# Optimization experiments

Hardware: AMD Instinct MI355X
Metric: run time of the kernel (lower is better)

The kernel has to match this reference:

```python
import jax, jax.numpy as jnp
import numpy as np

N = 20000; E = 320000; G = 64; C_IN = 128; H = 128; L = 3; S = 4
EPS = 1e-5; SLOPE = 0.01  # GraphNorm eps, leaky_relu negative slope


def _kruskal(ei, ew, n):
    # Kruskal MST over edges sorted by usage-count weight; returns bidirectional MST edges
    # and the updated usage counts (used edges get +1), mirroring kruskal_mst_track_usage.
    order = np.argsort(ew, kind='stable')
    s = ei[0][order]; d = ei[1][order]
    parent = np.arange(n)
    def find(u):
        while parent[u] != u:
            parent[u] = parent[parent[u]]
            u = parent[u]
        return u
    mst = []; used = []
    for i in range(s.shape[0]):
        ru = find(s[i]); rv = find(d[i])
        if ru != rv:
            parent[ru] = rv
            mst.append((s[i], d[i]))
            used.append(order[i])
            if len(mst) == n - 1:
                break
    ew = ew.copy(); ew[np.asarray(used)] += 1
    m = np.asarray(mst, dtype=np.int64).T  # [2, ~n-1]
    return np.concatenate([m, m[::-1]], axis=1), ew  # bidirectional


def setup_inputs():
    rng = np.random.default_rng(0)
    x = rng.standard_normal((N, C_IN), dtype=np.float32)
    edge_index = rng.integers(0, N, size=(2, E)).astype(np.int64)
    batch = np.sort(rng.integers(0, G, size=N)).astype(np.int64)
    # split_graph: shuffle edges, then repeatedly extract MSTs (no_grad / CPU in original)
    perm = rng.permutation(E)
    ei_p = edge_index[:, perm]
    ew = np.zeros(E, dtype=np.int64)
    msts = []
    for _ in range(S - 1):  # only splits 0..3 are used; split 0 is the shuffled full graph
        m, ew = _kruskal(ei_p, ew, N)
        msts.append(m)
    def gp(shape):
        return jnp.asarray((0.05 * rng.standard_normal(shape)).astype(np.float32))
    return {
        'x': jnp.asarray(x),
        'emb_W': gp((C_IN, H)), 'emb_b': gp((H,)),
        'main_W': gp((L, H, H)), 'main_b': gp((L, H)),
        'main_gw': jnp.ones((L, H), jnp.float32), 'main_gb': jnp.zeros((L, H), jnp.float32), 'main_gms': jnp.ones((L, H), jnp.float32),
        'loc_W': gp((L, H, H)), 'loc_b': gp((L, H)),
        'loc_gw': jnp.ones((L, H), jnp.float32), 'loc_gb': jnp.zeros((L, H), jnp.float32), 'loc_gms': jnp.ones((L, H), jnp.float32),
        'merge_W': gp((H * (S + 1), H)), 'merge_b': gp((H,)),
        'edge_index': jnp.asarray(edge_index),
        'edges0': jnp.asarray(ei_p),
        'edges1': jnp.asarray(msts[0]),
        'edges2': jnp.asarray(msts[1]),
        'edges3': jnp.asarray(msts[2]),
        'batch': jnp.asarray(batch),
    }


def _seg(v, idx, n):
    return jax.ops.segment_sum(v, idx, num_segments=n)


def _gcn(x, W, b, src, dst):
    # PyG GCNConv with self-loops and symmetric normalization
    n = x.shape[0]
    h = x @ W
    deg = _seg(jnp.ones(src.shape[0], x.dtype), dst, n) + 1.0
    dinv = jax.lax.rsqrt(deg)
    coef = (dinv[src] * dinv[dst])[:, None]
    out = _seg(h[src] * coef, dst, n) + h * (dinv * dinv)[:, None]  # neighbors + self-loop
    return out + b


def _graph_norm(x, batch, cnt, w, b, ms):
    # PyG GraphNorm: per-graph mean with learnable mean_scale, per-graph variance
    mean = _seg(x, batch, G) / cnt
    out = x - ms * mean[batch]
    var = _seg(out * out, batch, G) / cnt
    inv = jax.lax.rsqrt(var + EPS)
    return w * out * inv[batch] + b


def _gnn(x, src, dst, Ws, bs, gw, gb, gms, batch, cnt):
    hist = []
    for l in range(L):
        x = _gcn(x, Ws[l], bs[l], src, dst)
        x = _graph_norm(x, batch, cnt, gw[l], gb[l], gms[l])
        x = jax.nn.leaky_relu(x, SLOPE)
        hist.append(x)  # dropout in eval mode = identity
    return hist


def _forward(x, emb_W, emb_b, main_W, main_b, main_gw, main_gb, main_gms,
             loc_W, loc_b, loc_gw, loc_gb, loc_gms, merge_W, merge_b,
             edge_index, edges0, edges1, edges2, edges3, batch):
    cnt = jnp.maximum(_seg(jnp.ones(N, x.dtype), batch, G), 1.0)[:, None]  # [G,1]
    h = x @ emb_W + emb_b
    main_hist = _gnn(h, edge_index[0], edge_index[1], main_W, main_b, main_gw, main_gb, main_gms, batch, cnt)
    split_hists = [_gnn(h, e[0], e[1], loc_W, loc_b, loc_gw, loc_gb, loc_gms, batch, cnt)
                   for e in (edges0, edges1, edges2, edges3)]
    gs = []
    for l in range(L):
        xl = jnp.concatenate([sh[l] for sh in split_hists] + [main_hist[l]], axis=1)  # [N, 5H]
        xl = xl @ merge_W + merge_b
        gs.append(_seg(xl, batch, G) / cnt)  # global_mean_pool
    return jnp.mean(jnp.stack(gs), axis=0)  # [G, H]


def reference(x, emb_W, emb_b, main_W, main_b, main_gw, main_gb, main_gms,
              loc_W, loc_b, loc_gw, loc_gb, loc_gms, merge_W, merge_b,
              edge_index, edges0, edges1, edges2, edges3, batch):
    return _forward(x, emb_W, emb_b, main_W, main_b, main_gw, main_gb, main_gms,
                    loc_W, loc_b, loc_gw, loc_gb, loc_gms, merge_W, merge_b,
                    edge_index, edges0, edges1, edges2, edges3, batch)
```

## Files before the change

### kernel.cpp

```cpp
#include <hip/hip_runtime.h>

#define NN 20000
#define NNP 20032
#define NH 128
#define NG 64
#define NLAY 3
#define NCH 5
#define GEPS 1e-5f
#define GSLOPE 0.01f

typedef unsigned short u16;
typedef unsigned int u32;
typedef __attribute__((ext_vector_type(8))) short short8;
typedef __attribute__((ext_vector_type(4))) float float4v;
typedef __attribute__((ext_vector_type(2))) float f32x2;

__device__ __forceinline__ u16 f2bf(float f) {
  union { float f; u32 u; } v; v.f = f;
  u32 r = (v.u + 0x7fffu + ((v.u >> 16) & 1u)) >> 16;
  return (u16)r;
}

struct ZP {
  const u16* A[NCH];
  const u16* W[NCH];
  u16* Y[NCH];
  int ystride[NCH];
  u16* Xo[NCH];
  u16* Xn[NCH];
  const float* bias[NCH];
  const float* gw[NCH];
  const float* gb[NCH];
  const float* gms[NCH];
  int colbase[NCH];
};

struct ES4 {
  const int* e[4];
  int cnt[4];
  int off[4];
};


__global__ void k_deg(ES4 es, int* __restrict__ deg) {
  int s = blockIdx.y;
  int i = blockIdx.x * 256 + threadIdx.x;
  int E = es.cnt[s];
  if (i < E) atomicAdd(&deg[s * NN + es.e[s][E + i]], 1);
}

__global__ __launch_bounds__(1024) void k_scan(const int* __restrict__ deg,
                                               int* __restrict__ indptr,
                                               int* __restrict__ cursor,
                                               float* __restrict__ dinv,
                                               const int* __restrict__ batch,
                                               int* __restrict__ counts,
                                               int* __restrict__ gstart) {
  int s = blockIdx.x;
  int t = threadIdx.x;
  if (s == 4) {
    int g = t;
    if (g < NG) {
      auto lb = [&](int key) {
        int lo = 0, hi = NN;
        while (lo < hi) {
          int mid = (lo + hi) >> 1;
          if (batch[mid] < key) lo = mid + 1; else hi = mid;
        }
        return lo;
      };
      int a = lb(g), b = lb(g + 1);
      gstart[g] = a;
      counts[g] = b - a;
    }
    return;
  }
  const int* d = deg + s * NN;
  int* ip = indptr + s * (NN + 1);
  int* cu = cursor + s * (NN + 1);
  int lane = t & 63, wv = t >> 6;
  __shared__ int wsum[16];
  int run = 0;
  const int NT = (NN + 1023) / 1024;
  for (int tile = 0; tile < NT; tile++) {
    int idx = tile * 1024 + t;
    int v = 0;
    if (idx < NN) {
      v = d[idx];
      dinv[s * NN + idx] = rsqrtf((float)v + 1.0f);
    }
    int x = v;
#pragma unroll
    for (int o = 1; o < 64; o <<= 1) {
      int y = __shfl_up(x, o);
      if (lane >= o) x += y;
    }
    if (lane == 63) wsum[wv] = x;
    __syncthreads();
    if (wv == 0) {
      int y = (lane < 16) ? wsum[lane] : 0;
#pragma unroll
      for (int o = 1; o < 16; o <<= 1) {
        int z = __shfl_up(y, o);
        if (lane >= o) y += z;
      }
      if (lane < 16) wsum[lane] = y;
    }
    __syncthreads();
    int waveoff = (wv == 0) ? 0 : wsum[wv - 1];
    int excl = run + waveoff + x - v;
    if (idx < NN) { ip[idx] = excl; cu[idx] = excl; }
    run += wsum[15];
    __syncthreads();
  }
  if (t == 0) { ip[NN] = run; cu[NN] = run; }
}

__global__ void k_fill(ES4 es, const float* __restrict__ dinv, int* __restrict__ cursor,
                       int2* __restrict__ ent) {
  int s = blockIdx.y;
  int i = blockIdx.x * 256 + threadIdx.x;
  int E = es.cnt[s];
  if (i >= E) return;
  int src = es.e[s][i];
  int dst = es.e[s][E + i];
  int pos = atomicAdd(&cursor[s * (NN + 1) + dst], 1);
  float c = dinv[s * NN + src] * dinv[s * NN + dst];
  ent[es.off[s] + pos] = make_int2(src, __float_as_int(c));
}

__global__ __launch_bounds__(256) void k_prep(const float* __restrict__ embW,
                                              const float* __restrict__ locW,
                                              const float* __restrict__ mainW,
                                              u16* __restrict__ wt,
                                              const float* __restrict__ x,
                                              u16* __restrict__ xb) {
  int ybk = blockIdx.y;
  if (ybk == 7) {
    int i = (blockIdx.x * 256 + threadIdx.x) * 8;
    if (i >= NN * NH) return;
    float4 a = *(const float4*)(x + i);
    float4 b = *(const float4*)(x + i + 4);
    uint4 o;
    o.x = f2bf(a.x) | ((u32)f2bf(a.y) << 16);
    o.y = f2bf(a.z) | ((u32)f2bf(a.w) << 16);
    o.z = f2bf(b.x) | ((u32)f2bf(b.y) << 16);
    o.w = f2bf(b.z) | ((u32)f2bf(b.w) << 16);
    *(uint4*)(xb + i) = o;
    return;
  }
  if (blockIdx.x >= 16) return;
  int mat = ybk;
  const float* W = (mat == 0) ? embW : ((mat <= 3) ? locW + (mat - 1) * NH * NH
                                                   : mainW + (mat - 4) * NH * NH);
  int tile = blockIdx.x;
  int tk = (tile >> 2) * 32;
  int tn = (tile & 3) * 32;
  __shared__ float tl[32][33];
  int c = threadIdx.x & 31, r = threadIdx.x >> 5;
#pragma unroll
  for (int rr = 0; rr < 32; rr += 8)
    tl[r + rr][c] = W[(size_t)(tk + r + rr) * NH + tn + c];
  __syncthreads();
#pragma unroll
  for (int rr = 0; rr < 32; rr += 8)
    wt[(size_t)mat * NH * NH + (size_t)(tn + r + rr) * NH + tk + c] = f2bf(tl[c][r + rr]);
}


__global__ __launch_bounds__(256) void k_gemm_bf(ZP p, const float* __restrict__ gbias) {
  int zi = blockIdx.y;
  const u16* __restrict__ A = p.A[zi];
  const u16* __restrict__ Wt = p.W[zi];
  u16* __restrict__ Y = p.Y[zi];
  int yst = p.ystride[zi];
  __shared__ u16 As[64][136];
  __shared__ u16 Bs[128][136];
  int t = threadIdx.x;
  int row0 = blockIdx.x * 64;
  int c = t & 15, rs = t >> 4;
#pragma unroll
  for (int pass = 0; pass < 4; pass++) {
    int r = pass * 16 + rs;
    *(uint4*)(&As[r][c * 8]) = *(const uint4*)(A + (size_t)(row0 + r) * NH + c * 8);
  }
#pragma unroll
  for (int pass = 0; pass < 8; pass++) {
    int n = pass * 16 + rs;
    *(uint4*)(&Bs[n][c * 8]) = *(const uint4*)(Wt + (size_t)n * NH + c * 8);
  }
  __syncthreads();
  int lane = t & 63, w = t >> 6;
  int m16 = lane & 15, quad = lane >> 4;
  float4v acc[8];
#pragma unroll
  for (int i = 0; i < 8; i++) acc[i] = (float4v)(0.f);
#pragma unroll
  for (int kk = 0; kk < 4; kk++) {
    short8 av = *(const short8*)(&As[w * 16 + m16][kk * 32 + quad * 8]);
#pragma unroll
    for (int ct = 0; ct < 8; ct++) {
      short8 bv = *(const short8*)(&Bs[ct * 16 + m16][kk * 32 + quad * 8]);
      acc[ct] = __builtin_amdgcn_mfma_f32_16x16x32_bf16(av, bv, acc[ct], 0, 0, 0);
    }
  }
  __syncthreads();
#pragma unroll
  for (int ct = 0; ct < 8; ct++) {
    float bv = gbias ? gbias[ct * 16 + m16] : 0.f;
#pragma unroll
    for (int r = 0; r < 4; r++) {
      As[w * 16 + quad * 4 + r][ct * 16 + m16] = f2bf(acc[ct][r] + bv);
    }
  }
  __syncthreads();
#pragma unroll
  for (int pass = 0; pass < 4; pass++) {
    int r = pass * 16 + rs;
    int gr = row0 + r;
    if (gr < NN) *(uint4*)(Y + (size_t)gr * yst + c * 8) = *(const uint4*)(&As[r][c * 8]);
  }
}

__device__ __forceinline__ f32x2 bf2x2(u32 v) {
  f32x2 r;
  r.x = __uint_as_float(v << 16);
  r.y = __uint_as_float(v & 0xffff0000u);
  return r;
}

__device__ __forceinline__ void fma8p(f32x2* a, uint4 v, float cf) {
  f32x2 c2; c2.x = cf; c2.y = cf;
  a[0] += c2 * bf2x2(v.x);
  a[1] += c2 * bf2x2(v.y);
  a[2] += c2 * bf2x2(v.z);
  a[3] += c2 * bf2x2(v.w);
}

__device__ __forceinline__ void fin_chain(const float* a, const u16* Yb, int st, int node,
                                          int fo, float d2, const float* bias,
                                          u16* __restrict__ Xo) {
  uint4 sv = *(const uint4*)(Yb + (size_t)node * st + fo);
  float s[8] = {
    __uint_as_float(sv.x << 16), __uint_as_float(sv.x & 0xffff0000u),
    __uint_as_float(sv.y << 16), __uint_as_float(sv.y & 0xffff0000u),
    __uint_as_float(sv.z << 16), __uint_as_float(sv.z & 0xffff0000u),
    __uint_as_float(sv.w << 16), __uint_as_float(sv.w & 0xffff0000u)};
  float4 b0 = *(const float4*)(bias + fo);
  float4 b1 = *(const float4*)(bias + fo + 4);
  float bb[8] = {b0.x, b0.y, b0.z, b0.w, b1.x, b1.y, b1.z, b1.w};
  float o[8];
#pragma unroll
  for (int j = 0; j < 8; j++) o[j] = a[j] + d2 * s[j] + bb[j];
  uint4 ou;
  u32* op = (u32*)&ou;
#pragma unroll
  for (int j = 0; j < 4; j++)
    op[j] = (u32)f2bf(o[2 * j]) | ((u32)f2bf(o[2 * j + 1]) << 16);
  *(uint4*)(Xo + (size_t)node * NH + fo) = ou;
}

__global__ __launch_bounds__(256) void k_agg2(ZP p, const int* __restrict__ indptr,
                                              const int2* __restrict__ ent,
                                              const float* __restrict__ dinv, int4 entoff) {
  int y = blockIdx.y;
  int wv = threadIdx.x >> 6, lane = threadIdx.x & 63;
  int g = lane >> 4;
  int fo = (lane & 15) * 8;
  if (y == 0) {
    int node = blockIdx.x * 4 + wv;
    if (node >= NN) return;
    int beg = indptr[node], end = indptr[node + 1];
    const u16* __restrict__ Y0 = p.Y[0];
    const u16* __restrict__ Y4 = p.Y[4];
    int st = p.ystride[0];
    f32x2 a0[4], a4[4];
#pragma unroll
    for (int j = 0; j < 4; j++) { a0[j] = (f32x2)(0.f); a4[j] = (f32x2)(0.f); }
    int e = beg + g;
    for (; e + 4 < end; e += 8) {
      int2 sa = ent[e];
      int2 sb = ent[e + 4];
      size_t ra = (size_t)sa.x * st + fo;
      size_t rb = (size_t)sb.x * st + fo;
      uint4 va0 = *(const uint4*)(Y0 + ra);
      uint4 va4 = *(const uint4*)(Y4 + ra);
      uint4 vb0 = *(const uint4*)(Y0 + rb);
      uint4 vb4 = *(const uint4*)(Y4 + rb);
      float ca = __int_as_float(sa.y), cb = __int_as_float(sb.y);
      fma8p(a0, va0, ca); fma8p(a4, va4, ca);
      fma8p(a0, vb0, cb); fma8p(a4, vb4, cb);
    }
    if (e < end) {
      int2 sc = ent[e];
      float cf = __int_as_float(sc.y);
      size_t ro = (size_t)sc.x * st + fo;
      uint4 v0 = *(const uint4*)(Y0 + ro);
      uint4 v4 = *(const uint4*)(Y4 + ro);
      fma8p(a0, v0, cf);
      fma8p(a4, v4, cf);
    }
    float* f0 = (float*)a0;
    float* f4 = (float*)a4;
#pragma unroll
    for (int j = 0; j < 8; j++) {
      f0[j] += __shfl_xor(f0[j], 16);
      f0[j] += __shfl_xor(f0[j], 32);
      f4[j] += __shfl_xor(f4[j], 16);
      f4[j] += __shfl_xor(f4[j], 32);
    }
    if (g == 0) {
      float di = dinv[node];
      float d2 = di * di;
      fin_chain(f0, Y0, st, node, fo, d2, p.bias[0], p.Xo[0]);
      fin_chain(f4, Y4, st, node, fo, d2, p.bias[4], p.Xo[4]);
    }
  } else {
    int node = blockIdx.x * 16 + wv * 4 + g;
    if (node >= NN) return;
    int s = y;
    const int* ip = indptr + s * (NN + 1);
    int eb = (s == 1) ? entoff.y : ((s == 2) ? entoff.z : entoff.w);
    const u16* __restrict__ Y = p.Y[y];
    int st = p.ystride[y];
    int beg = ip[node], end = ip[node + 1];
    const int2* __restrict__ ev = ent + eb;
    f32x2 a[4];
#pragma unroll
    for (int j = 0; j < 4; j++) a[j] = (f32x2)(0.f);
    for (int e = beg; e < end; e++) {
      int2 sc = ev[e];
      uint4 v = *(const uint4*)(Y + (size_t)sc.x * st + fo);
      fma8p(a, v, __int_as_float(sc.y));
    }
    float di = dinv[s * NN + node];
    float d2 = di * di;
    fin_chain((float*)a, Y, st, node, fo, d2, p.bias[y], p.Xo[y]);
  }
}

__global__ __launch_bounds__(256) void k_norm2(ZP p, const int* __restrict__ gstart,
                                               const int* __restrict__ counts,
                                               float* __restrict__ Ml) {
  int g = blockIdx.x, zi = blockIdx.y, fc = blockIdx.z;
  const u16* __restrict__ X = p.Xo[zi];
  u16* __restrict__ Xn = p.Xn[zi];
  int t = threadIdx.x;
  int fj = t & 15;
  int f2 = fc * 32 + fj * 2;
  int rh = t >> 4;
  int start = gstart[g], cnt = counts[g];
  __shared__ float red[4][16][17];
  float s0 = 0.f, s1 = 0.f, q0 = 0.f, q1 = 0.f;
  for (int i = rh; i < cnt; i += 16) {
    u32 v = *(const u32*)(X + (size_t)(start + i) * NH + f2);
    float v0 = __uint_as_float(v << 16), v1 = __uint_as_float(v & 0xffff0000u);
    s0 += v0; q0 += v0 * v0;
    s1 += v1; q1 += v1 * v1;
  }
  red[0][rh][fj] = s0; red[1][rh][fj] = s1;
  red[2][rh][fj] = q0; red[3][rh][fj] = q1;
  __syncthreads();
#pragma unroll
  for (int off = 8; off >= 1; off >>= 1) {
    if (rh < off) {
      red[0][rh][fj] += red[0][rh + off][fj];
      red[1][rh][fj] += red[1][rh + off][fj];
      red[2][rh][fj] += red[2][rh + off][fj];
      red[3][rh][fj] += red[3][rh + off][fj];
    }
    __syncthreads();
  }
  float cntf = fmaxf((float)cnt, 1.f);
  float w0 = p.gw[zi][f2], w1 = p.gw[zi][f2 + 1];
  float b0 = p.gb[zi][f2], b1 = p.gb[zi][f2 + 1];
  float ms0 = p.gms[zi][f2], ms1 = p.gms[zi][f2 + 1];
  float mean0 = red[0][0][fj] / cntf, mean1 = red[1][0][fj] / cntf;
  float var0 = red[2][0][fj] / cntf - (2.f * ms0 - ms0 * ms0) * mean0 * mean0;
  float var1 = red[3][0][fj] / cntf - (2.f * ms1 - ms1 * ms1) * mean1 * mean1;
  float inv0 = rsqrtf(var0 + GEPS), inv1 = rsqrtf(var1 + GEPS);
  __syncthreads();
  float m0 = 0.f, m1 = 0.f;
  for (int i = rh; i < cnt; i += 16) {
    size_t ro = (size_t)(start + i) * NH + f2;
    u32 v = *(const u32*)(X + ro);
    float v0 = __uint_as_float(v << 16), v1 = __uint_as_float(v & 0xffff0000u);
    float o0 = w0 * (v0 - ms0 * mean0) * inv0 + b0;
    float o1 = w1 * (v1 - ms1 * mean1) * inv1 + b1;
    o0 = (o0 >= 0.f) ? o0 : GSLOPE * o0;
    o1 = (o1 >= 0.f) ? o1 : GSLOPE * o1;
    if (Xn) *(u32*)(Xn + ro) = (u32)f2bf(o0) | ((u32)f2bf(o1) << 16);
    m0 += o0; m1 += o1;
  }
  red[0][rh][fj] = m0; red[1][rh][fj] = m1;
  __syncthreads();
#pragma unroll
  for (int off = 8; off >= 1; off >>= 1) {
    if (rh < off) {
      red[0][rh][fj] += red[0][rh + off][fj];
      red[1][rh][fj] += red[1][rh + off][fj];
    }
    __syncthreads();
  }
  if (rh == 0) {
    int col = p.colbase[zi] + f2;
    Ml[(size_t)g * 640 + col] = red[0][0][fj];
    Ml[(size_t)g * 640 + col + 1] = red[1][0][fj];
  }
}

__global__ __launch_bounds__(256) void k_mergeout(const float* __restrict__ M,
                                                  const float* __restrict__ mergeW,
                                                  const float* __restrict__ mergeb,
                                                  const int* __restrict__ counts,
                                                  float* __restrict__ out) {
  int g = blockIdx.x;
  int f = threadIdx.x & 127, h = threadIdx.x >> 7;
  __shared__ float mrow[640];
  __shared__ float red[128];
  float acc = 0.f;
  for (int l = 0; l < NLAY; l++) {
    const float* Mr = M + ((size_t)l * NG + g) * 640;
    for (int i = threadIdx.x; i < 640; i += 256) mrow[i] = Mr[i];
    __syncthreads();
    float s = 0.f;
    int k0 = h * 320;
#pragma unroll 8
    for (int k = k0; k < k0 + 320; k++) s += mrow[k] * mergeW[(size_t)k * NH + f];
    if (h) red[f] = s;
    __syncthreads();
    if (!h) acc += s + red[f];
    __syncthreads();
  }
  if (!h) {
    float cnt = fmaxf((float)counts[g], 1.f);
    out[(size_t)g * NH + f] = acc / (3.f * cnt) + mergeb[f];
  }
}


struct Offs {
  size_t counts, gstart, deg, M, dinv, indptr, cursor, ent, wt, xbf, h0, ydual;
  size_t yb[NCH], xo[NCH], xn[NCH];
  size_t memset1_off, memset1_len, total;
};

static size_t build_offs(Offs& o, int Etot) {
  size_t off = 0;
  auto alloc = [&](size_t bytes) -> size_t {
    off = (off + 255) & ~(size_t)255;
    size_t s = off;
    off += bytes;
    return s;
  };
  o.counts = alloc(NG * 4);
  o.gstart = alloc(NG * 4);
  o.deg = alloc((size_t)4 * NN * 4);
  o.memset1_off = o.deg;
  o.memset1_len = (size_t)4 * NN * 4;
  o.M = alloc((size_t)NLAY * NG * 640 * 4);
  o.dinv = alloc((size_t)4 * NN * 4);
  o.indptr = alloc((size_t)4 * (NN + 1) * 4);
  o.cursor = alloc((size_t)4 * (NN + 1) * 4);
  o.ent = alloc((size_t)Etot * 8);
  o.wt = alloc((size_t)7 * NH * NH * 2);
  o.xbf = alloc((size_t)NNP * NH * 2);
  o.h0 = alloc((size_t)NNP * NH * 2);
  o.ydual = alloc((size_t)NN * 256 * 2);
  for (int i = 1; i < 4; i++) o.yb[i] = alloc((size_t)NN * NH * 2);
  for (int i = 0; i < NCH; i++) {
    o.xo[i] = alloc((size_t)NN * NH * 2);
    o.xn[i] = alloc((size_t)NNP * NH * 2);
  }
  o.total = off;
  return off;
}

extern "C" void kernel_launch(void* const* d_in, const int* in_sizes, int n_in,
                              void* d_out, int out_size, void* d_ws, size_t ws_size,
                              hipStream_t stream) {
  if (n_in < 21) return;
  const float* x = (const float*)d_in[0];
  const float* embW = (const float*)d_in[1];
  const float* embb = (const float*)d_in[2];
  const float* mainW = (const float*)d_in[3];
  const float* mainb = (const float*)d_in[4];
  const float* maingw = (const float*)d_in[5];
  const float* maingb = (const float*)d_in[6];
  const float* maingms = (const float*)d_in[7];
  const float* locW = (const float*)d_in[8];
  const float* locb = (const float*)d_in[9];
  const float* locgw = (const float*)d_in[10];
  const float* locgb = (const float*)d_in[11];
  const float* locgms = (const float*)d_in[12];
  const float* mergeW = (const float*)d_in[13];
  const float* mergeb = (const float*)d_in[14];
  const int* edge_index = (const int*)d_in[15];
  const int* edges1 = (const int*)d_in[17];
  const int* edges2 = (const int*)d_in[18];
  const int* edges3 = (const int*)d_in[19];
  const int* batch = (const int*)d_in[20];

  int E0 = in_sizes[15] / 2;
  int E1 = in_sizes[17] / 2, E2 = in_sizes[18] / 2, E3 = in_sizes[19] / 2;
  int Etot = E0 + E1 + E2 + E3;
  int maxE = E0 > E1 ? E0 : E1;
  maxE = maxE > E2 ? maxE : E2;
  maxE = maxE > E3 ? maxE : E3;

  Offs o;
  if (build_offs(o, Etot) > ws_size) return;

  char* ws = (char*)d_ws;
  int* counts = (int*)(ws + o.counts);
  int* gstart = (int*)(ws + o.gstart);
  int* deg = (int*)(ws + o.deg);
  float* M = (float*)(ws + o.M);
  float* dinv = (float*)(ws + o.dinv);
  int* indptr = (int*)(ws + o.indptr);
  int* cursor = (int*)(ws + o.cursor);
  int2* ent = (int2*)(ws + o.ent);
  u16* wt = (u16*)(ws + o.wt);
  u16* xbf = (u16*)(ws + o.xbf);
  u16* h0 = (u16*)(ws + o.h0);
  u16* ydual = (u16*)(ws + o.ydual);
  u16 *yb[NCH], *xo[NCH], *xn[NCH];
  for (int i = 1; i < 4; i++) yb[i] = (u16*)(ws + o.yb[i]);
  for (int i = 0; i < NCH; i++) {
    xo[i] = (u16*)(ws + o.xo[i]);
    xn[i] = (u16*)(ws + o.xn[i]);
  }

  ES4 es;
  es.e[0] = edge_index; es.e[1] = edges1; es.e[2] = edges2; es.e[3] = edges3;
  es.cnt[0] = E0; es.cnt[1] = E1; es.cnt[2] = E2; es.cnt[3] = E3;
  es.off[0] = 0; es.off[1] = E0; es.off[2] = E0 + E1; es.off[3] = E0 + E1 + E2;
  int4 entoff = make_int4(0, E0, E0 + E1, E0 + E1 + E2);

  hipMemsetAsync(ws + o.memset1_off, 0, o.memset1_len, stream);
  k_deg<<<dim3((maxE + 255) / 256, 4), 256, 0, stream>>>(es, deg);
  k_scan<<<5, 1024, 0, stream>>>(deg, indptr, cursor, dinv, batch, counts, gstart);
  k_fill<<<dim3((maxE + 255) / 256, 4), 256, 0, stream>>>(es, dinv, cursor, ent);
  k_prep<<<dim3((NN * NH / 8 + 255) / 256, 8), 256, 0, stream>>>(embW, locW, mainW, wt,
                                                                 x, xbf);

  const int nrb = (NN + 63) / 64;

  {
    ZP pe = {};
    pe.A[0] = xbf; pe.W[0] = wt; pe.Y[0] = h0; pe.ystride[0] = NH;
    k_gemm_bf<<<dim3(nrb, 1), 256, 0, stream>>>(pe, embb);
  }

  for (int l = 0; l < NLAY; l++) {
    ZP p = {};
    for (int zi = 0; zi < NCH; zi++) {
      bool isMain = (zi == 4);
      p.A[zi] = (l == 0) ? (const u16*)h0 : (const u16*)xn[zi];
      p.W[zi] = wt + (size_t)((isMain ? 4 : 1) + l) * NH * NH;
      if (zi == 0) { p.Y[0] = ydual; p.ystride[0] = 256; }
      else if (zi == 4) { p.Y[4] = ydual + 128; p.ystride[4] = 256; }
      else { p.Y[zi] = yb[zi]; p.ystride[zi] = 128; }
      p.Xo[zi] = xo[zi];
      p.Xn[zi] = (l == NLAY - 1) ? (u16*)nullptr : xn[zi];
      p.bias[zi] = (isMain ? mainb : locb) + (size_t)l * NH;
      p.gw[zi] = (isMain ? maingw : locgw) + (size_t)l * NH;
      p.gb[zi] = (isMain ? maingb : locgb) + (size_t)l * NH;
      p.gms[zi] = (isMain ? maingms : locgms) + (size_t)l * NH;
      p.colbase[zi] = isMain ? 512 : zi * NH;
    }
    if (l == 0) {
      ZP pg = {};
      pg.A[0] = h0; pg.W[0] = wt + (size_t)1 * NH * NH; pg.Y[0] = ydual; pg.ystride[0] = 256;
      pg.A[1] = h0; pg.W[1] = wt + (size_t)4 * NH * NH; pg.Y[1] = ydual + 128; pg.ystride[1] = 256;
      k_gemm_bf<<<dim3(nrb, 2), 256, 0, stream>>>(pg, (const float*)nullptr);
      p.Y[1] = ydual; p.Y[2] = ydual; p.Y[3] = ydual;
      p.ystride[1] = p.ystride[2] = p.ystride[3] = 256;
    } else {
      k_gemm_bf<<<dim3(nrb, NCH), 256, 0, stream>>>(p, (const float*)nullptr);
    }
    k_agg2<<<dim3(NN / 4, 4), 256, 0, stream>>>(p, indptr, ent, dinv, entoff);
    k_norm2<<<dim3(NG, NCH, 4), 256, 0, stream>>>(p, gstart, counts,
                                                  M + (size_t)l * NG * 640);
  }

  k_mergeout<<<NG, 256, 0, stream>>>(M, mergeW, mergeb, counts, (float*)d_out);
}
```

Baseline: 394.4 us.

## Pack CSR entries to 32-bit, flatten aggregation grid, fuse setup kernels

CSR entries shrink from an int2 (source index plus fp32 coefficient) to one 32-bit word holding a 16-bit source index and a bf16 coefficient. This halves index traffic in the aggregation loop. The aggregation launch becomes a flat 1D grid sized exactly for the main dual-channel part and the three split channels, so the many blocks that used to exit immediately are no longer launched. The degree-count and weight/input preparation kernels are merged into one launch. The risks are bf16 rounding of the normalization coefficient and hardcoded block counts that assume N=20000 and the test edge counts.

```diff
diff --git a/kernel.cpp b/kernel.cpp
--- a/kernel.cpp
+++ b/kernel.cpp
@@ -41,13 +41,6 @@
   int off[4];
 };
 
-
-__global__ void k_deg(ES4 es, int* __restrict__ deg) {
-  int s = blockIdx.y;
-  int i = blockIdx.x * 256 + threadIdx.x;
-  int E = es.cnt[s];
-  if (i < E) atomicAdd(&deg[s * NN + es.e[s][E + i]], 1);
-}
 
 __global__ __launch_bounds__(1024) void k_scan(const int* __restrict__ deg,
                                                int* __restrict__ indptr,
@@ -117,7 +110,7 @@
 }
 
 __global__ void k_fill(ES4 es, const float* __restrict__ dinv, int* __restrict__ cursor,
-                       int2* __restrict__ ent) {
+                       u32* __restrict__ ent) {
   int s = blockIdx.y;
   int i = blockIdx.x * 256 + threadIdx.x;
   int E = es.cnt[s];
@@ -126,17 +119,25 @@
   int dst = es.e[s][E + i];
   int pos = atomicAdd(&cursor[s * (NN + 1) + dst], 1);
   float c = dinv[s * NN + src] * dinv[s * NN + dst];
-  ent[es.off[s] + pos] = make_int2(src, __float_as_int(c));
-}
-
-__global__ __launch_bounds__(256) void k_prep(const float* __restrict__ embW,
-                                              const float* __restrict__ locW,
-                                              const float* __restrict__ mainW,
-                                              u16* __restrict__ wt,
-                                              const float* __restrict__ x,
-                                              u16* __restrict__ xb) {
+  ent[es.off[s] + pos] = (u32)src | ((u32)f2bf(c) << 16);
+}
+
+__global__ __launch_bounds__(256) void k_setup(ES4 es, int* __restrict__ deg,
+                                               const float* __restrict__ embW,
+                                               const float* __restrict__ locW,
+                                               const float* __restrict__ mainW,
+                                               u16* __restrict__ wt,
+                                               const float* __restrict__ x,
+                                               u16* __restrict__ xb) {
   int ybk = blockIdx.y;
-  if (ybk == 7) {
+  if (ybk < 4) {
+    int s = ybk;
+    int i = blockIdx.x * 256 + threadIdx.x;
+    int E = es.cnt[s];
+    if (i < E) atomicAdd(&deg[s * NN + es.e[s][E + i]], 1);
+    return;
+  }
+  if (ybk == 11) {
     int i = (blockIdx.x * 256 + threadIdx.x) * 8;
     if (i >= NN * NH) return;
     float4 a = *(const float4*)(x + i);
@@ -150,7 +151,7 @@
     return;
   }
   if (blockIdx.x >= 16) return;
-  int mat = ybk;
+  int mat = ybk - 4;
   const float* W = (mat == 0) ? embW : ((mat <= 3) ? locW + (mat - 1) * NH * NH
                                                    : mainW + (mat - 4) * NH * NH);
   int tile = blockIdx.x;
@@ -261,15 +262,14 @@
 }
 
 __global__ __launch_bounds__(256) void k_agg2(ZP p, const int* __restrict__ indptr,
-                                              const int2* __restrict__ ent,
+                                              const u32* __restrict__ ent,
                                               const float* __restrict__ dinv, int4 entoff) {
-  int y = blockIdx.y;
+  int b = blockIdx.x;
   int wv = threadIdx.x >> 6, lane = threadIdx.x & 63;
   int g = lane >> 4;
   int fo = (lane & 15) * 8;
-  if (y == 0) {
-    int node = blockIdx.x * 4 + wv;
-    if (node >= NN) return;
+  if (b < 5000) {
+    int node = b * 4 + wv;
     int beg = indptr[node], end = indptr[node + 1];
     const u16* __restrict__ Y0 = p.Y[0];
     const u16* __restrict__ Y4 = p.Y[4];
@@ -279,22 +279,23 @@
     for (int j = 0; j < 4; j++) { a0[j] = (f32x2)(0.f); a4[j] = (f32x2)(0.f); }
     int e = beg + g;
     for (; e + 4 < end; e += 8) {
-      int2 sa = ent[e];
-      int2 sb = ent[e + 4];
-      size_t ra = (size_t)sa.x * st + fo;
-      size_t rb = (size_t)sb.x * st + fo;
+      u32 sa = ent[e];
+      u32 sb = ent[e + 4];
+      size_t ra = (size_t)(sa & 0xffffu) * st + fo;
+      size_t rb = (size_t)(sb & 0xffffu) * st + fo;
       uint4 va0 = *(const uint4*)(Y0 + ra);
       uint4 va4 = *(const uint4*)(Y4 + ra);
       uint4 vb0 = *(const uint4*)(Y0 + rb);
       uint4 vb4 = *(const uint4*)(Y4 + rb);
-      float ca = __int_as_float(sa.y), cb = __int_as_float(sb.y);
+      float ca = __uint_as_float(sa & 0xffff0000u);
+      float cb = __uint_as_float(sb & 0xffff0000u);
       fma8p(a0, va0, ca); fma8p(a4, va4, ca);
       fma8p(a0, vb0, cb); fma8p(a4, vb4, cb);
     }
     if (e < end) {
-      int2 sc = ent[e];
-      float cf = __int_as_float(sc.y);
-      size_t ro = (size_t)sc.x * st + fo;
+      u32 sc = ent[e];
+      float cf = __uint_as_float(sc & 0xffff0000u);
+      size_t ro = (size_t)(sc & 0xffffu) * st + fo;
       uint4 v0 = *(const uint4*)(Y0 + ro);
       uint4 v4 = *(const uint4*)(Y4 + ro);
       fma8p(a0, v0, cf);
@@ -316,26 +317,26 @@
       fin_chain(f4, Y4, st, node, fo, d2, p.bias[4], p.Xo[4]);
     }
   } else {
-    int node = blockIdx.x * 16 + wv * 4 + g;
-    if (node >= NN) return;
-    int s = y;
+    int mb = b - 5000;
+    int s = 1 + mb / 1250;
+    int node = (mb % 1250) * 16 + wv * 4 + g;
     const int* ip = indptr + s * (NN + 1);
     int eb = (s == 1) ? entoff.y : ((s == 2) ? entoff.z : entoff.w);
-    const u16* __restrict__ Y = p.Y[y];
-    int st = p.ystride[y];
+    const u16* __restrict__ Y = p.Y[s];
+    int st = p.ystride[s];
     int beg = ip[node], end = ip[node + 1];
-    const int2* __restrict__ ev = ent + eb;
+    const u32* __restrict__ ev = ent + eb;
     f32x2 a[4];
 #pragma unroll
     for (int j = 0; j < 4; j++) a[j] = (f32x2)(0.f);
     for (int e = beg; e < end; e++) {
-      int2 sc = ev[e];
-      uint4 v = *(const uint4*)(Y + (size_t)sc.x * st + fo);
-      fma8p(a, v, __int_as_float(sc.y));
+      u32 sc = ev[e];
+      uint4 v = *(const uint4*)(Y + (size_t)(sc & 0xffffu) * st + fo);
+      fma8p(a, v, __uint_as_float(sc & 0xffff0000u));
     }
     float di = dinv[s * NN + node];
     float d2 = di * di;
-    fin_chain((float*)a, Y, st, node, fo, d2, p.bias[y], p.Xo[y]);
+    fin_chain((float*)a, Y, st, node, fo, d2, p.bias[s], p.Xo[s]);
   }
 }
 
@@ -462,7 +463,7 @@
   o.dinv = alloc((size_t)4 * NN * 4);
   o.indptr = alloc((size_t)4 * (NN + 1) * 4);
   o.cursor = alloc((size_t)4 * (NN + 1) * 4);
-  o.ent = alloc((size_t)Etot * 8);
+  o.ent = alloc((size_t)Etot * 4);
   o.wt = alloc((size_t)7 * NH * NH * 2);
   o.xbf = alloc((size_t)NNP * NH * 2);
   o.h0 = alloc((size_t)NNP * NH * 2);
@@ -519,7 +520,7 @@
   float* dinv = (float*)(ws + o.dinv);
   int* indptr = (int*)(ws + o.indptr);
   int* cursor = (int*)(ws + o.cursor);
-  int2* ent = (int2*)(ws + o.ent);
+  u32* ent = (u32*)(ws + o.ent);
   u16* wt = (u16*)(ws + o.wt);
   u16* xbf = (u16*)(ws + o.xbf);
   u16* h0 = (u16*)(ws + o.h0);
@@ -538,11 +539,10 @@
   int4 entoff = make_int4(0, E0, E0 + E1, E0 + E1 + E2);
 
   hipMemsetAsync(ws + o.memset1_off, 0, o.memset1_len, stream);
-  k_deg<<<dim3((maxE + 255) / 256, 4), 256, 0, stream>>>(es, deg);
+  k_setup<<<dim3((maxE + 255) / 256, 12), 256, 0, stream>>>(es, deg, embW, locW, mainW,
+                                                            wt, x, xbf);
   k_scan<<<5, 1024, 0, stream>>>(deg, indptr, cursor, dinv, batch, counts, gstart);
   k_fill<<<dim3((maxE + 255) / 256, 4), 256, 0, stream>>>(es, dinv, cursor, ent);
-  k_prep<<<dim3((NN * NH / 8 + 255) / 256, 8), 256, 0, stream>>>(embW, locW, mainW, wt,
-                                                                 x, xbf);
 
   const int nrb = (NN + 63) / 64;
 
@@ -579,7 +579,7 @@
     } else {
       k_gemm_bf<<<dim3(nrb, NCH), 256, 0, stream>>>(p, (const float*)nullptr);
     }
-    k_agg2<<<dim3(NN / 4, 4), 256, 0, stream>>>(p, indptr, ent, dinv, entoff);
+    k_agg2<<<8750, 256, 0, stream>>>(p, indptr, ent, dinv, entoff);
     k_norm2<<<dim3(NG, NCH, 4), 256, 0, stream>>>(p, gstart, counts,
                                                   M + (size_t)l * NG * 640);
   }
```

Result: faster. 385.3 us (-2.3%).
